# Optimization experiments

Measured on AMD Instinct MI355X. Metric: run time of the kernel, lower is better.

Reference implementation:

```python
import jax, jax.numpy as jnp
import numpy as np

HEAD_DIM = 256
ROPE_THETA = 1000000.0
EPS = 1e-6


def rmsnorm(x, w):
    # torch.nn.RMSNorm: x / sqrt(mean(x^2) + eps) * w, over last dim
    var = jnp.mean(jnp.square(x), axis=-1, keepdims=True)
    return x * jax.lax.rsqrt(var + EPS) * w


def apply_rope(x):
    # x: [b, h, L, head_dim]; rotate-half-split RoPE as in the source
    L, hd = x.shape[-2], x.shape[-1]
    half = hd // 2
    pos = jnp.arange(L, dtype=x.dtype)
    idx = jnp.arange(half, dtype=x.dtype)
    inv_freq = 1.0 / (ROPE_THETA ** (2.0 * idx / hd))
    freqs = pos[:, None] * inv_freq[None, :]          # [L, half]
    cos = jnp.cos(freqs)[None, None]                  # [1,1,L,half]
    sin = jnp.sin(freqs)[None, None]
    x1, x2 = x[..., :half], x[..., half:]
    return jnp.concatenate([x1 * cos - x2 * sin, x1 * sin + x2 * cos], axis=-1)


def setup_inputs() -> dict:
    key = jax.random.key(0)
    ks = jax.random.split(key, 7)
    B, L, D = 2, 2048, 2048
    H, HD = 8, HEAD_DIM
    s = lambda fan_in: 1.0 / np.sqrt(fan_in)
    return {
        "x": jax.random.normal(ks[0], (B, L, D), jnp.float32),
        "q_proj": jax.random.normal(ks[1], (H * HD, D), jnp.float32) * s(D),
        "k_proj": jax.random.normal(ks[2], (HD, D), jnp.float32) * s(D),
        "v_proj": jax.random.normal(ks[3], (HD, D), jnp.float32) * s(D),
        "o_proj": jax.random.normal(ks[4], (D, H * HD), jnp.float32) * s(H * HD),
        "q_norm": jnp.ones((HD,), jnp.float32),
        "k_norm": jnp.ones((HD,), jnp.float32),
    }


def reference(x, q_proj, k_proj, v_proj, o_proj, q_norm, k_norm):
    B, L, D = x.shape
    HD = k_proj.shape[0]
    H = q_proj.shape[0] // HD

    # projections (Linear weight is [out, in])
    k = rmsnorm(x @ k_proj.T, k_norm)                 # [B, L, HD]
    q = rmsnorm((x @ q_proj.T).reshape(B, L, H, HD), q_norm)
    v = x @ v_proj.T                                  # [B, L, HD]

    q = q.transpose(0, 2, 1, 3)                       # [B, H, L, HD]
    k = k[:, None]                                    # [B, 1, L, HD] (MQA)
    v = v[:, None]

    q = apply_rope(q)
    k = apply_rope(k)

    scores = jnp.matmul(q, jnp.swapaxes(k, -1, -2)) / jnp.sqrt(
        jnp.asarray(256.0, x.dtype))                  # [B, H, L, L]
    causal = jnp.tril(jnp.ones((L, L), bool))
    scores = jnp.where(causal, scores, -jnp.inf)
    w = jax.nn.softmax(scores, axis=-1)
    ctx = jnp.matmul(w, v)                            # [B, H, L, HD]
    ctx = ctx.transpose(0, 2, 1, 3).reshape(B, L, H * HD)
    return ctx @ o_proj.T
```

## Files before the change

kernel.cpp:

```cpp
#include <hip/hip_runtime.h>
#include <hip/hip_bf16.h>
#include <stdint.h>

typedef __bf16 bf16;
typedef bf16 bf16x8 __attribute__((ext_vector_type(8)));
typedef float f32x4 __attribute__((ext_vector_type(4)));

__device__ __forceinline__ bf16x8 load8(const float* p) {
    const f32x4 lo = *(const f32x4*)p;
    const f32x4 hi = *(const f32x4*)(p + 4);
    bf16x8 v;
#pragma unroll
    for (int r = 0; r < 4; ++r) { v[r] = (bf16)lo[r]; v[4 + r] = (bf16)hi[r]; }
    return v;
}
__device__ __forceinline__ bf16x8 load8(const bf16* p) {
    return *(const bf16x8*)p;
}

__device__ __forceinline__ void gload16(const bf16* g, bf16* l) {
    __builtin_amdgcn_global_load_lds((const __attribute__((address_space(1))) void*)g,
                                     (__attribute__((address_space(3))) void*)l, 16, 0, 0);
}

__global__ __launch_bounds__(256) void cvt_bf16(const float* __restrict__ src,
                                                bf16* __restrict__ dst, int n8) {
    int idx = blockIdx.x * 256 + threadIdx.x;
    const int stride = gridDim.x * 256;
    for (; idx < n8; idx += stride) {
        const f32x4 lo = *(const f32x4*)(src + (size_t)idx * 8);
        const f32x4 hi = *(const f32x4*)(src + (size_t)idx * 8 + 4);
        bf16x8 v;
#pragma unroll
        for (int r = 0; r < 4; ++r) { v[r] = (bf16)lo[r]; v[4 + r] = (bf16)hi[r]; }
        *(bf16x8*)(dst + (size_t)idx * 8) = v;
    }
}

__global__ __launch_bounds__(256) void cvt_qkvx(const float* __restrict__ x,
                                                const float* __restrict__ q,
                                                const float* __restrict__ k,
                                                const float* __restrict__ v,
                                                bf16* __restrict__ dst,
                                                int nx8, int nq8, int nk8, int nv8) {
    const int total = nx8 + nq8 + nk8 + nv8;
    int idx = blockIdx.x * 256 + threadIdx.x;
    const int stride = gridDim.x * 256;
    for (; idx < total; idx += stride) {
        const float* s;
        int off;
        if (idx < nx8)                   { s = x; off = idx; }
        else if (idx < nx8 + nq8)        { s = q; off = idx - nx8; }
        else if (idx < nx8 + nq8 + nk8)  { s = k; off = idx - nx8 - nq8; }
        else                             { s = v; off = idx - nx8 - nq8 - nk8; }
        const f32x4 lo = *(const f32x4*)(s + (size_t)off * 8);
        const f32x4 hi = *(const f32x4*)(s + (size_t)off * 8 + 4);
        bf16x8 o;
#pragma unroll
        for (int r = 0; r < 4; ++r) { o[r] = (bf16)lo[r]; o[4 + r] = (bf16)hi[r]; }
        *(bf16x8*)(dst + (size_t)idx * 8) = o;
    }
}

template <typename AT, typename BT, typename CT>
__global__ __launch_bounds__(256) void gemm_bt(const AT* __restrict__ A,
                                               const BT* __restrict__ B,
                                               CT* __restrict__ C,
                                               int M, int N, int K) {
    __shared__ __align__(16) bf16 As[128 * 32];
    __shared__ __align__(16) bf16 Bs[128 * 32];
    const int tid  = threadIdx.x;
    const int wave = tid >> 6, lane = tid & 63;
    const int quad = lane >> 4, l16 = lane & 15;
    const int m0 = blockIdx.y * 128, n0 = blockIdx.x * 128;
    const int wr = (wave >> 1) * 64, wc = (wave & 1) * 64;

    const int srow = wave * 32 + (lane >> 2);
    const int scol = (lane & 3) * 8;
    const AT* Ag = A + (size_t)(m0 + srow) * K + scol;
    const BT* Bg = B + (size_t)(n0 + srow) * K + scol;
    bf16* Asw = &As[srow * 32 + scol];
    bf16* Bsw = &Bs[srow * 32 + scol];

    f32x4 acc[4][4] = {};

    for (int k0 = 0; k0 < K; k0 += 32) {
        const bf16x8 av0 = load8(Ag + k0);
        const bf16x8 av1 = load8(Ag + k0 + (size_t)16 * K);
        const bf16x8 bv0 = load8(Bg + k0);
        const bf16x8 bv1 = load8(Bg + k0 + (size_t)16 * K);
        __syncthreads();
        *(bf16x8*)(Asw)           = av0;
        *(bf16x8*)(Asw + 16 * 32) = av1;
        *(bf16x8*)(Bsw)           = bv0;
        *(bf16x8*)(Bsw + 16 * 32) = bv1;
        __syncthreads();

        bf16x8 a[4], b[4];
#pragma unroll
        for (int i = 0; i < 4; ++i)
            a[i] = *(const bf16x8*)&As[(wr + i * 16 + l16) * 32 + quad * 8];
#pragma unroll
        for (int j = 0; j < 4; ++j)
            b[j] = *(const bf16x8*)&Bs[(wc + j * 16 + l16) * 32 + quad * 8];
#pragma unroll
        for (int i = 0; i < 4; ++i)
#pragma unroll
            for (int j = 0; j < 4; ++j)
                acc[i][j] = __builtin_amdgcn_mfma_f32_16x16x32_bf16(a[i], b[j], acc[i][j], 0, 0, 0);
    }

#pragma unroll
    for (int i = 0; i < 4; ++i)
#pragma unroll
        for (int j = 0; j < 4; ++j) {
            const int row = m0 + wr + i * 16 + quad * 4;
            const int col = n0 + wc + j * 16 + l16;
#pragma unroll
            for (int r = 0; r < 4; ++r)
                C[(size_t)(row + r) * N + col] = (CT)acc[i][j][r];
        }
}

template <typename CT>
__global__ __launch_bounds__(256) void gemm_bb(const bf16* __restrict__ A,
                                               const bf16* __restrict__ B,
                                               CT* __restrict__ C,
                                               int M, int N, int K) {
    __shared__ __align__(16) bf16 As[128 * 32];
    __shared__ __align__(16) bf16 Bs[128 * 32];
    const int tid  = threadIdx.x;
    const int wave = tid >> 6, lane = tid & 63;
    const int quad = lane >> 4, l16 = lane & 15;
    const int m0 = blockIdx.y * 128, n0 = blockIdx.x * 128;
    const int wr = (wave >> 1) * 64, wc = (wave & 1) * 64;

    const int srow = tid >> 2, scol = (tid & 3) * 8;
    const bf16* Ag = A + (size_t)(m0 + srow) * K + scol;
    const bf16* Bg = B + (size_t)(n0 + srow) * K + scol;
    bf16* Adst = As + wave * 512;
    bf16* Bdst = Bs + wave * 512;

    f32x4 acc[4][4] = {};

    for (int k0 = 0; k0 < K; k0 += 32) {
        __syncthreads();
        gload16(Ag + k0, Adst);
        gload16(Ag + k0 + (size_t)64 * K, Adst + 2048);
        gload16(Bg + k0, Bdst);
        gload16(Bg + k0 + (size_t)64 * K, Bdst + 2048);
        __syncthreads();

        bf16x8 a[4], b[4];
#pragma unroll
        for (int i = 0; i < 4; ++i)
            a[i] = *(const bf16x8*)&As[(wr + i * 16 + l16) * 32 + quad * 8];
#pragma unroll
        for (int j = 0; j < 4; ++j)
            b[j] = *(const bf16x8*)&Bs[(wc + j * 16 + l16) * 32 + quad * 8];
#pragma unroll
        for (int i = 0; i < 4; ++i)
#pragma unroll
            for (int j = 0; j < 4; ++j)
                acc[i][j] = __builtin_amdgcn_mfma_f32_16x16x32_bf16(a[i], b[j], acc[i][j], 0, 0, 0);
    }

#pragma unroll
    for (int i = 0; i < 4; ++i)
#pragma unroll
        for (int j = 0; j < 4; ++j) {
            const int row = m0 + wr + i * 16 + quad * 4;
            const int col = n0 + wc + j * 16 + l16;
#pragma unroll
            for (int r = 0; r < 4; ++r)
                C[(size_t)(row + r) * N + col] = (CT)acc[i][j][r];
        }
}

__global__ __launch_bounds__(256) void gemm_qkv(const bf16* __restrict__ A,
                                                const bf16* __restrict__ W,
                                                bf16* __restrict__ Cq,
                                                bf16* __restrict__ Ck,
                                                bf16* __restrict__ Cv,
                                                int M, int K) {
    __shared__ __align__(16) bf16 As[128 * 32];
    __shared__ __align__(16) bf16 Bs[128 * 32];
    const int tid  = threadIdx.x;
    const int wave = tid >> 6, lane = tid & 63;
    const int quad = lane >> 4, l16 = lane & 15;
    const int m0 = blockIdx.y * 128, n0 = blockIdx.x * 128;
    const int wr = (wave >> 1) * 64, wc = (wave & 1) * 64;

    const int srow = tid >> 2, scol = (tid & 3) * 8;
    const bf16* Ag = A + (size_t)(m0 + srow) * K + scol;
    const bf16* Bg = W + (size_t)(n0 + srow) * K + scol;
    bf16* Adst = As + wave * 512;
    bf16* Bdst = Bs + wave * 512;

    f32x4 acc[4][4] = {};

    for (int k0 = 0; k0 < K; k0 += 32) {
        __syncthreads();
        gload16(Ag + k0, Adst);
        gload16(Ag + k0 + (size_t)64 * K, Adst + 2048);
        gload16(Bg + k0, Bdst);
        gload16(Bg + k0 + (size_t)64 * K, Bdst + 2048);
        __syncthreads();

        bf16x8 a[4], b[4];
#pragma unroll
        for (int i = 0; i < 4; ++i)
            a[i] = *(const bf16x8*)&As[(wr + i * 16 + l16) * 32 + quad * 8];
#pragma unroll
        for (int j = 0; j < 4; ++j)
            b[j] = *(const bf16x8*)&Bs[(wc + j * 16 + l16) * 32 + quad * 8];
#pragma unroll
        for (int i = 0; i < 4; ++i)
#pragma unroll
            for (int j = 0; j < 4; ++j)
                acc[i][j] = __builtin_amdgcn_mfma_f32_16x16x32_bf16(a[i], b[j], acc[i][j], 0, 0, 0);
    }

    bf16* cb; int cw, coff;
    if (n0 < 2048)      { cb = Cq; cw = 2048; coff = 0; }
    else if (n0 < 2304) { cb = Ck; cw = 256;  coff = 2048; }
    else                { cb = Cv; cw = 256;  coff = 2304; }

#pragma unroll
    for (int i = 0; i < 4; ++i)
#pragma unroll
        for (int j = 0; j < 4; ++j) {
            const int row = m0 + wr + i * 16 + quad * 4;
            const int col = n0 + wc + j * 16 + l16 - coff;
#pragma unroll
            for (int r = 0; r < 4; ++r)
                cb[(size_t)(row + r) * cw + col] = (bf16)acc[i][j][r];
        }
}

__device__ __forceinline__ void norm_rope_body(bf16* __restrict__ x,
                                               const float* __restrict__ w,
                                               int rid, int L, int div, int t) {
    const size_t base = (size_t)rid * 256;
    const float v = (float)x[base + t];
    float ss = v * v;
#pragma unroll
    for (int off = 32; off >= 1; off >>= 1) ss += __shfl_xor(ss, off);

    __shared__ float wsum[4];
    __shared__ float buf[256];
    const int wave = t >> 6, lane = t & 63;
    if (lane == 0) wsum[wave] = ss;
    __syncthreads();
    const float var = (wsum[0] + wsum[1] + wsum[2] + wsum[3]) * (1.0f / 256.0f);
    const float inv = rsqrtf(var + 1e-6f);
    buf[t] = v * inv * w[t];
    __syncthreads();

    const int pos = (rid / div) % L;
    const int i = t & 127;
    const float freq = (float)pos * exp2f(-(float)i * (19.93156857f / 128.0f));
    const float c = cosf(freq), s = sinf(freq);
    const float x1 = buf[i], x2 = buf[i + 128];
    const float out = (t < 128) ? (x1 * c - x2 * s) : (x1 * s + x2 * c);
    x[base + t] = (bf16)out;
}

__global__ __launch_bounds__(256) void norm_rope(bf16* __restrict__ x,
                                                 const float* __restrict__ w,
                                                 int L, int div) {
    norm_rope_body(x, w, blockIdx.x, L, div, threadIdx.x);
}

__global__ __launch_bounds__(256) void norm_rope2(bf16* __restrict__ Q,
                                                  bf16* __restrict__ K,
                                                  const float* __restrict__ qw,
                                                  const float* __restrict__ kw,
                                                  int L, int MH) {
    const int row = blockIdx.x;
    if (row < MH) norm_rope_body(Q, qw, row, L, 8, threadIdx.x);
    else          norm_rope_body(K, kw, row - MH, L, 1, threadIdx.x);
}

__global__ __launch_bounds__(256) void transpose_v(const bf16* __restrict__ V,
                                                   bf16* __restrict__ Vt, int L) {
    __shared__ bf16 tile[32][33];
    const int b = blockIdx.z;
    const int l0 = blockIdx.x * 32, d0 = blockIdx.y * 32;
    const int tx = threadIdx.x & 31, ty = threadIdx.x >> 5;
#pragma unroll
    for (int i = 0; i < 32; i += 8)
        tile[ty + i][tx] = V[((size_t)b * L + l0 + ty + i) * 256 + d0 + tx];
    __syncthreads();
#pragma unroll
    for (int i = 0; i < 32; i += 8)
        Vt[((size_t)b * 256 + d0 + ty + i) * L + l0 + tx] = tile[tx][ty + i];
}

__device__ __forceinline__ int kswz(int r, int c) { return r * 256 + (c ^ ((r & 7) << 3)); }
__device__ __forceinline__ int vswz(int r, int c) { return r * 64  + (c ^ ((r & 7) << 3)); }

template <int SPLIT>
__global__ __launch_bounds__(256, 2) void flash_attn(const bf16* __restrict__ Q,
                                                     const bf16* __restrict__ K,
                                                     const bf16* __restrict__ Vt,
                                                     bf16* __restrict__ Ctx,
                                                     float* __restrict__ P0,
                                                     float* __restrict__ P1,
                                                     float* __restrict__ ML0,
                                                     float* __restrict__ ML1, int L) {
    constexpr int H = 8, HD = 256;
    extern __shared__ __align__(16) bf16 smem[];
    bf16* Ks = smem;
    bf16* Vs = Ks + 64 * 256;
    bf16* Ps = Vs + 256 * 64;

    const int z = blockIdx.x, h = blockIdx.y;
    const int b    = SPLIT ? ((int)blockIdx.z >> 1) : (int)blockIdx.z;
    const int half = SPLIT ? ((int)blockIdx.z & 1) : 0;
    const int tid = threadIdx.x;
    const int wave = tid >> 6, lane = tid & 63;
    const int quad = lane >> 4, l16 = lane & 15;
    const int nqt = L / 64;

    const bf16* Kb = K + (size_t)b * L * HD;
    const bf16* Vb = Vt + (size_t)b * HD * L;
    bf16* Pw = Ps + wave * 16 * 64;

    const int krow = tid >> 5, kcol = (tid & 31) * 8;
    const int vrow = tid >> 3, vcol = (tid & 7) * 8;
    const int kcs = kcol ^ ((krow & 7) << 3);
    const int vcs = vcol ^ ((vrow & 7) << 3);
    bf16* kdst = Ks + wave * 512;
    bf16* vdst = Vs + wave * 512;

    for (int pass = 0; pass < 2; ++pass) {
        const int qt = pass ? z : (nqt - 1 - z);
        const int q0 = qt * 64 + wave * 16;
        const int s  = qt + 1;
        const int c0 = (s + 1) >> 1;
        const int kt0 = (SPLIT && half) ? c0 : 0;
        const int cnt = SPLIT ? (half ? s - c0 : c0) : s;

        bf16x8 qf[8];
        {
            const bf16* qbase = Q + ((size_t)(b * L + q0 + l16) * H + h) * HD + quad * 8;
#pragma unroll
            for (int kc = 0; kc < 8; ++kc) qf[kc] = *(const bf16x8*)(qbase + kc * 32);
        }

        f32x4 Oacc[16] = {};
        float mrow[4], lrow[4];
#pragma unroll
        for (int r = 0; r < 4; ++r) { mrow[r] = -1e30f; lrow[r] = 0.0f; }

        __syncthreads();
        if (cnt > 0) {
            const int kv0 = kt0 * 64;
#pragma unroll
            for (int i = 0; i < 8; ++i)
                gload16(Kb + (size_t)(kv0 + i * 8 + krow) * HD + kcs, kdst + i * 2048);
#pragma unroll
            for (int i = 0; i < 8; ++i)
                gload16(Vb + (size_t)(i * 32 + vrow) * L + kv0 + vcs, vdst + i * 2048);
        }
        __syncthreads();

        for (int it = 0; it < cnt; ++it) {
            const int kt = kt0 + it;
            const int kv0 = kt * 64;
            const int nv0 = kv0 + 64;
            const bool more = (it + 1 < cnt);

            f32x4 S[4];
#pragma unroll
            for (int nt = 0; nt < 4; ++nt) {
                f32x4 slo = {0.f, 0.f, 0.f, 0.f}, shi = {0.f, 0.f, 0.f, 0.f};
                const int krw = nt * 16 + l16;
#pragma unroll
                for (int kc = 0; kc < 4; ++kc)
                    slo = __builtin_amdgcn_mfma_f32_16x16x32_bf16(qf[kc], *(const bf16x8*)&Ks[kswz(krw, quad * 8 + kc * 32)], slo, 0, 0, 0);
#pragma unroll
                for (int kc = 4; kc < 8; ++kc)
                    shi = __builtin_amdgcn_mfma_f32_16x16x32_bf16(qf[kc], *(const bf16x8*)&Ks[kswz(krw, quad * 8 + kc * 32)], shi, 0, 0, 0);
                S[nt] = slo + shi;
            }

            __syncthreads();
            if (more) {
#pragma unroll
                for (int i = 0; i < 8; ++i)
                    gload16(Kb + (size_t)(nv0 + i * 8 + krow) * HD + kcs, kdst + i * 2048);
            }

            float rowmax[4] = {-1e30f, -1e30f, -1e30f, -1e30f};
            const bool diag = (kt == qt);
#pragma unroll
            for (int nt = 0; nt < 4; ++nt) {
                const int col = kv0 + nt * 16 + l16;
#pragma unroll
                for (int r = 0; r < 4; ++r) {
                    float sv = S[nt][r] * 0.0625f;
                    if (diag && col > q0 + quad * 4 + r) sv = -1e30f;
                    S[nt][r] = sv;
                    rowmax[r] = fmaxf(rowmax[r], sv);
                }
            }
#pragma unroll
            for (int off = 1; off < 16; off <<= 1)
#pragma unroll
                for (int r = 0; r < 4; ++r)
                    rowmax[r] = fmaxf(rowmax[r], __shfl_xor(rowmax[r], off));

            float alpha[4], rsum[4];
#pragma unroll
            for (int r = 0; r < 4; ++r) {
                const float mnew = fmaxf(mrow[r], rowmax[r]);
                alpha[r] = __expf(mrow[r] - mnew);
                mrow[r] = mnew;
                rsum[r] = 0.0f;
            }
#pragma unroll
            for (int nt = 0; nt < 4; ++nt)
#pragma unroll
                for (int r = 0; r < 4; ++r) {
                    const float p = __expf(S[nt][r] - mrow[r]);
                    rsum[r] += p;
                    Pw[vswz(quad * 4 + r, nt * 16 + l16)] = (bf16)p;
                }
#pragma unroll
            for (int off = 1; off < 16; off <<= 1)
#pragma unroll
                for (int r = 0; r < 4; ++r) rsum[r] += __shfl_xor(rsum[r], off);
#pragma unroll
            for (int r = 0; r < 4; ++r) lrow[r] = lrow[r] * alpha[r] + rsum[r];

#pragma unroll
            for (int nt = 0; nt < 16; ++nt)
#pragma unroll
                for (int r = 0; r < 4; ++r) Oacc[nt][r] *= alpha[r];

            bf16x8 pf[2];
#pragma unroll
            for (int ks = 0; ks < 2; ++ks)
                pf[ks] = *(const bf16x8*)&Pw[vswz(l16, ks * 32 + quad * 8)];
#pragma unroll
            for (int nt = 0; nt < 16; ++nt) {
                const int vrw = nt * 16 + l16;
                f32x4 o = Oacc[nt];
#pragma unroll
                for (int ks = 0; ks < 2; ++ks)
                    o = __builtin_amdgcn_mfma_f32_16x16x32_bf16(pf[ks], *(const bf16x8*)&Vs[vswz(vrw, ks * 32 + quad * 8)], o, 0, 0, 0);
                Oacc[nt] = o;
            }

            __syncthreads();
            if (more) {
#pragma unroll
                for (int i = 0; i < 8; ++i)
                    gload16(Vb + (size_t)(i * 32 + vrow) * L + nv0 + vcs, vdst + i * 2048);
            }
        }

        if (SPLIT) {
            float* Pd  = half ? P1 : P0;
            float* MLd = half ? ML1 : ML0;
            const size_t rowbase = (((size_t)b * H + h) * nqt + qt) * 64 + wave * 16;
            float* prow = Pd + rowbase * 256;
#pragma unroll
            for (int nt = 0; nt < 16; ++nt)
#pragma unroll
                for (int r = 0; r < 4; ++r)
                    prow[(size_t)(quad * 4 + r) * 256 + nt * 16 + l16] = Oacc[nt][r];
            if (l16 == 0) {
#pragma unroll
                for (int r = 0; r < 4; ++r) {
                    const size_t rr = rowbase + quad * 4 + r;
                    MLd[rr * 2 + 0] = mrow[r];
                    MLd[rr * 2 + 1] = lrow[r];
                }
            }
        } else {
            bf16* obase = Ctx + ((size_t)(b * L + q0) * H + h) * HD;
#pragma unroll
            for (int nt = 0; nt < 16; ++nt)
#pragma unroll
                for (int r = 0; r < 4; ++r) {
                    const float val = Oacc[nt][r] / lrow[r];
                    obase[(size_t)(quad * 4 + r) * (H * HD) + nt * 16 + l16] = (bf16)val;
                }
        }
    }
}

__global__ __launch_bounds__(256) void merge_partials(const float* __restrict__ P0,
                                                      const float* __restrict__ P1,
                                                      const float* __restrict__ ML0,
                                                      const float* __restrict__ ML1,
                                                      bf16* __restrict__ Ctx, int L) {
    constexpr int H = 8, HD = 256;
    const int qt = blockIdx.x, h = blockIdx.y, b = blockIdx.z;
    const int nqt = L / 64;
    const int t = threadIdx.x;
    const size_t rowbase = (((size_t)b * H + h) * nqt + qt) * 64;
    const int rlo = t >> 6;
    const int d = (t & 63) * 4;
#pragma unroll
    for (int it = 0; it < 16; ++it) {
        const int r = it * 4 + rlo;
        const size_t rr = rowbase + r;
        const float m0 = ML0[rr * 2], l0 = ML0[rr * 2 + 1];
        const float m1 = ML1[rr * 2], l1 = ML1[rr * 2 + 1];
        const float mn = fmaxf(m0, m1);
        const float a0 = __expf(m0 - mn), a1 = __expf(m1 - mn);
        const float linv = 1.0f / (l0 * a0 + l1 * a1);
        const f32x4 o0 = *(const f32x4*)&P0[rr * 256 + d];
        const f32x4 o1 = *(const f32x4*)&P1[rr * 256 + d];
        bf16* op = Ctx + ((size_t)(b * L + qt * 64 + r) * H + h) * HD + d;
#pragma unroll
        for (int j = 0; j < 4; ++j) op[j] = (bf16)((o0[j] * a0 + o1[j] * a1) * linv);
    }
}

extern "C" void kernel_launch(void* const* d_in, const int* in_sizes, int n_in,
                              void* d_out, int out_size, void* d_ws, size_t ws_size,
                              hipStream_t stream) {
    const float* x      = (const float*)d_in[0];
    const float* q_proj = (const float*)d_in[1];
    const float* k_proj = (const float*)d_in[2];
    const float* v_proj = (const float*)d_in[3];
    const float* o_proj = (const float*)d_in[4];
    const float* q_norm = (const float*)d_in[5];
    const float* k_norm = (const float*)d_in[6];
    float* out = (float*)d_out;

    constexpr int B = 2, L = 2048, D = 2048, H = 8, HD = 256;
    constexpr int M = B * L;
    constexpr int NQT = L / 64;
    constexpr int NQKV = D + 2 * HD;
    constexpr int FLASH_LDS = (64 * 256 + 256 * 64 + 4 * 16 * 64) * 2;

    static bool attr_set = false;
    if (!attr_set) {
        (void)hipFuncSetAttribute((const void*)flash_attn<0>,
                                  hipFuncAttributeMaxDynamicSharedMemorySize, FLASH_LDS);
        (void)hipFuncSetAttribute((const void*)flash_attn<1>,
                                  hipFuncAttributeMaxDynamicSharedMemorySize, FLASH_LDS);
        attr_set = true;
    }

    bf16* Qw  = (bf16*)d_ws;
    bf16* Kw  = Qw  + (size_t)M * D;
    bf16* Vw  = Kw  + (size_t)M * HD;
    bf16* Vtw = Vw  + (size_t)M * HD;
    bf16* Ctx = Vtw + (size_t)M * HD;

    char* region = (char*)(Ctx + (size_t)M * D);
    bf16* Xb   = (bf16*)region;
    bf16* Wqkv = Xb + (size_t)M * D;
    constexpr size_t PELEMS  = (size_t)B * H * NQT * 64 * 256;
    constexpr size_t MLELEMS = (size_t)B * H * NQT * 64 * 2;
    float* P0  = (float*)region;
    float* P1  = P0 + PELEMS;
    float* ML0 = P1 + PELEMS;
    float* ML1 = ML0 + MLELEMS;
    bf16*  Ob  = (bf16*)region;
    const size_t ws_needed = (size_t)((char*)(ML1 + MLELEMS) - (char*)d_ws);

    if (ws_size >= ws_needed) {
        cvt_qkvx<<<2048, 256, 0, stream>>>(x, q_proj, k_proj, v_proj, Xb,
                                           M * D / 8, D * D / 8, HD * D / 8, HD * D / 8);
        gemm_qkv<<<dim3(NQKV / 128, M / 128), 256, 0, stream>>>(Xb, Wqkv, Qw, Kw, Vw, M, D);
        norm_rope2<<<M * H + M, 256, 0, stream>>>(Qw, Kw, q_norm, k_norm, L, M * H);
        transpose_v<<<dim3(L / 32, HD / 32, B), 256, 0, stream>>>(Vw, Vtw, L);
        flash_attn<1><<<dim3(L / 128, H, B * 2), 256, FLASH_LDS, stream>>>(Qw, Kw, Vtw, Ctx,
                                                                           P0, P1, ML0, ML1, L);
        merge_partials<<<dim3(NQT, H, B), 256, 0, stream>>>(P0, P1, ML0, ML1, Ctx, L);
        cvt_bf16<<<2048, 256, 0, stream>>>(o_proj, Ob, D * D / 8);
        gemm_bb<float><<<dim3(D / 128, M / 128), 256, 0, stream>>>(Ctx, Ob, out, M, D, D);
    } else {
        gemm_bt<float, float, bf16><<<dim3(D / 128, M / 128), 256, 0, stream>>>(x, q_proj, Qw, M, D, D);
        gemm_bt<float, float, bf16><<<dim3(HD / 128, M / 128), 256, 0, stream>>>(x, k_proj, Kw, M, HD, D);
        gemm_bt<float, float, bf16><<<dim3(HD / 128, M / 128), 256, 0, stream>>>(x, v_proj, Vw, M, HD, D);
        norm_rope<<<M * H, 256, 0, stream>>>(Qw, q_norm, L, H);
        norm_rope<<<M, 256, 0, stream>>>(Kw, k_norm, L, 1);
        transpose_v<<<dim3(L / 32, HD / 32, B), 256, 0, stream>>>(Vw, Vtw, L);
        flash_attn<0><<<dim3(L / 128, H, B), 256, FLASH_LDS, stream>>>(Qw, Kw, Vtw, Ctx,
                                                                       P0, P1, ML0, ML1, L);
        gemm_bt<bf16, float, float><<<dim3(D / 128, M / 128), 256, 0, stream>>>(Ctx, o_proj, out, M, D, D);
    }
}
```

Measured before the change: 354.6 us.

## Swizzle GEMM block order, precompute RoPE table, raise MFMA priority in attention

Three separate changes. The two GEMM kernels remap block indices so consecutive workgroups spread across eight groups, aiming at better L2/XCD locality. A new kernel builds a cos/sin table once per call, and the fused norm+rope kernel reads from it instead of evaluating transcendentals per element. The flash attention MFMA loops are wrapped in s_setprio to favour the matrix work over other waves. The table is written into the workspace region Xb/Wqkv, which is dead after the QKV GEMM, and P0 reuses the same region later. The pos mask assumes L is a power of two.

```diff
diff --git a/kernel.cpp b/kernel.cpp
--- a/kernel.cpp
+++ b/kernel.cpp
@@ -132,7 +132,11 @@
     const int tid  = threadIdx.x;
     const int wave = tid >> 6, lane = tid & 63;
     const int quad = lane >> 4, l16 = lane & 15;
-    const int m0 = blockIdx.y * 128, n0 = blockIdx.x * 128;
+    const int nx = gridDim.x;
+    const int flat = blockIdx.y * nx + blockIdx.x;
+    const int cpx = (nx * gridDim.y) >> 3;
+    const int swz = (flat & 7) * cpx + (flat >> 3);
+    const int m0 = (swz / nx) * 128, n0 = (swz % nx) * 128;
     const int wr = (wave >> 1) * 64, wc = (wave & 1) * 64;
 
     const int srow = tid >> 2, scol = (tid & 3) * 8;
@@ -188,7 +192,11 @@
     const int tid  = threadIdx.x;
     const int wave = tid >> 6, lane = tid & 63;
     const int quad = lane >> 4, l16 = lane & 15;
-    const int m0 = blockIdx.y * 128, n0 = blockIdx.x * 128;
+    const int nx = gridDim.x;
+    const int flat = blockIdx.y * nx + blockIdx.x;
+    const int cpx = (nx * gridDim.y) >> 3;
+    const int swz = (flat & 7) * cpx + (flat >> 3);
+    const int m0 = (swz / nx) * 128, n0 = (swz % nx) * 128;
     const int wr = (wave >> 1) * 64, wc = (wave & 1) * 64;
 
     const int srow = tid >> 2, scol = (tid & 3) * 8;
@@ -238,9 +246,18 @@
         }
 }
 
-__device__ __forceinline__ void norm_rope_body(bf16* __restrict__ x,
+__global__ __launch_bounds__(256) void rope_table(float* __restrict__ ct) {
+    const int idx = blockIdx.x * 256 + threadIdx.x;
+    const int pos = idx >> 7, i = idx & 127;
+    const float freq = (float)pos * exp2f(-(float)i * (19.93156857f / 128.0f));
+    ct[idx * 2 + 0] = cosf(freq);
+    ct[idx * 2 + 1] = sinf(freq);
+}
+
+__device__ __forceinline__ void norm_rope_core(bf16* __restrict__ x,
                                                const float* __restrict__ w,
-                                               int rid, int L, int div, int t) {
+                                               int rid, int t,
+                                               float c, float s) {
     const size_t base = (size_t)rid * 256;
     const float v = (float)x[base + t];
     float ss = v * v;
@@ -257,29 +274,36 @@
     buf[t] = v * inv * w[t];
     __syncthreads();
 
+    const int i = t & 127;
+    const float x1 = buf[i], x2 = buf[i + 128];
+    const float out = (t < 128) ? (x1 * c - x2 * s) : (x1 * s + x2 * c);
+    x[base + t] = (bf16)out;
+}
+
+__global__ __launch_bounds__(256) void norm_rope(bf16* __restrict__ x,
+                                                 const float* __restrict__ w,
+                                                 int L, int div) {
+    const int rid = blockIdx.x, t = threadIdx.x;
     const int pos = (rid / div) % L;
     const int i = t & 127;
     const float freq = (float)pos * exp2f(-(float)i * (19.93156857f / 128.0f));
-    const float c = cosf(freq), s = sinf(freq);
-    const float x1 = buf[i], x2 = buf[i + 128];
-    const float out = (t < 128) ? (x1 * c - x2 * s) : (x1 * s + x2 * c);
-    x[base + t] = (bf16)out;
-}
-
-__global__ __launch_bounds__(256) void norm_rope(bf16* __restrict__ x,
-                                                 const float* __restrict__ w,
-                                                 int L, int div) {
-    norm_rope_body(x, w, blockIdx.x, L, div, threadIdx.x);
+    norm_rope_core(x, w, rid, t, cosf(freq), sinf(freq));
 }
 
 __global__ __launch_bounds__(256) void norm_rope2(bf16* __restrict__ Q,
                                                   bf16* __restrict__ K,
                                                   const float* __restrict__ qw,
                                                   const float* __restrict__ kw,
+                                                  const float* __restrict__ ct,
                                                   int L, int MH) {
-    const int row = blockIdx.x;
-    if (row < MH) norm_rope_body(Q, qw, row, L, 8, threadIdx.x);
-    else          norm_rope_body(K, kw, row - MH, L, 1, threadIdx.x);
+    const int row = blockIdx.x, t = threadIdx.x;
+    bf16* x; const float* w; int rid, pos;
+    if (row < MH) { x = Q; w = qw; rid = row;      pos = (rid >> 3) & (L - 1); }
+    else          { x = K; w = kw; rid = row - MH; pos = rid & (L - 1); }
+    const int i = t & 127;
+    const float c = ct[(pos * 128 + i) * 2 + 0];
+    const float s = ct[(pos * 128 + i) * 2 + 1];
+    norm_rope_core(x, w, rid, t, c, s);
 }
 
 __global__ __launch_bounds__(256) void transpose_v(const bf16* __restrict__ V,
@@ -373,6 +397,7 @@
             const bool more = (it + 1 < cnt);
 
             f32x4 S[4];
+            __builtin_amdgcn_s_setprio(1);
 #pragma unroll
             for (int nt = 0; nt < 4; ++nt) {
                 f32x4 slo = {0.f, 0.f, 0.f, 0.f}, shi = {0.f, 0.f, 0.f, 0.f};
@@ -385,6 +410,7 @@
                     shi = __builtin_amdgcn_mfma_f32_16x16x32_bf16(qf[kc], *(const bf16x8*)&Ks[kswz(krw, quad * 8 + kc * 32)], shi, 0, 0, 0);
                 S[nt] = slo + shi;
             }
+            __builtin_amdgcn_s_setprio(0);
 
             __syncthreads();
             if (more) {
@@ -444,6 +470,7 @@
 #pragma unroll
             for (int ks = 0; ks < 2; ++ks)
                 pf[ks] = *(const bf16x8*)&Pw[vswz(l16, ks * 32 + quad * 8)];
+            __builtin_amdgcn_s_setprio(1);
 #pragma unroll
             for (int nt = 0; nt < 16; ++nt) {
                 const int vrw = nt * 16 + l16;
@@ -453,6 +480,7 @@
                     o = __builtin_amdgcn_mfma_f32_16x16x32_bf16(pf[ks], *(const bf16x8*)&Vs[vswz(vrw, ks * 32 + quad * 8)], o, 0, 0, 0);
                 Oacc[nt] = o;
             }
+            __builtin_amdgcn_s_setprio(0);
 
             __syncthreads();
             if (more) {
@@ -558,6 +586,7 @@
     char* region = (char*)(Ctx + (size_t)M * D);
     bf16* Xb   = (bf16*)region;
     bf16* Wqkv = Xb + (size_t)M * D;
+    float* RT  = (float*)region;
     constexpr size_t PELEMS  = (size_t)B * H * NQT * 64 * 256;
     constexpr size_t MLELEMS = (size_t)B * H * NQT * 64 * 2;
     float* P0  = (float*)region;
@@ -571,7 +600,8 @@
         cvt_qkvx<<<2048, 256, 0, stream>>>(x, q_proj, k_proj, v_proj, Xb,
                                            M * D / 8, D * D / 8, HD * D / 8, HD * D / 8);
         gemm_qkv<<<dim3(NQKV / 128, M / 128), 256, 0, stream>>>(Xb, Wqkv, Qw, Kw, Vw, M, D);
-        norm_rope2<<<M * H + M, 256, 0, stream>>>(Qw, Kw, q_norm, k_norm, L, M * H);
+        rope_table<<<L * 128 / 256, 256, 0, stream>>>(RT);
+        norm_rope2<<<M * H + M, 256, 0, stream>>>(Qw, Kw, q_norm, k_norm, RT, L, M * H);
         transpose_v<<<dim3(L / 32, HD / 32, B), 256, 0, stream>>>(Vw, Vtw, L);
         flash_attn<1><<<dim3(L / 128, H, B * 2), 256, FLASH_LDS, stream>>>(Qw, Kw, Vtw, Ctx,
                                                                            P0, P1, ML0, ML1, L);
```

New measurement: 347.4 us. -2.0%, faster.
